# Performance work log

Measured on AMD Instinct MI355X. Metric: run time of the kernel, lower is better.

## Reference

```python
import jax, jax.numpy as jnp
import numpy as np

NEG_SLOPE = 0.2


def gat_conv(x, src, dst, W, a_src, a_dst, bias, heads, out_ch):
    # x: [N, F_in]; src/dst: [E] (message flows src -> dst, softmax over dst)
    N = x.shape[0]
    h = (x @ W).reshape(N, heads, out_ch)              # [N, H, C]
    alpha_s = (h * a_src).sum(-1)                      # [N, H]
    alpha_d = (h * a_dst).sum(-1)                      # [N, H]
    e = jax.nn.leaky_relu(alpha_s[src] + alpha_d[dst], NEG_SLOPE)  # [E, H]
    # segment softmax over destination nodes (every node has a self loop)
    emax = jax.ops.segment_max(e, dst, num_segments=N)             # [N, H]
    ee = jnp.exp(e - emax[dst])
    denom = jax.ops.segment_sum(ee, dst, num_segments=N)           # [N, H]
    alpha = ee / denom[dst]                                        # [E, H]
    msg = h[src] * alpha[..., None]                                # [E, H, C]
    out = jax.ops.segment_sum(msg, dst, num_segments=N)            # [N, H, C]
    return out.reshape(N, heads * out_ch) + bias


def setup_inputs() -> dict:
    key = jax.random.key(0)
    ks = jax.random.split(key, 12)
    N, E, EL = 100000, 1600000, 100000
    F_in, C, H = 128, 64, 2
    glorot = lambda k, shp: jax.random.normal(k, shp, jnp.float32) * np.sqrt(2.0 / (shp[0] + shp[-1]))
    return {
        "x": jax.random.normal(ks[0], (N, F_in), jnp.float32),
        "edge_index": jax.random.randint(ks[1], (2, E), 0, N, jnp.int32),
        "edge_label_index": jax.random.randint(ks[2], (2, EL), 0, N, jnp.int32),
        "W1": glorot(ks[3], (F_in, H * C)),
        "a_src1": glorot(ks[4], (H, C)),
        "a_dst1": glorot(ks[5], (H, C)),
        "b1": jnp.zeros((H * C,), jnp.float32),
        "W2": glorot(ks[6], (H * C, C)),
        "a_src2": glorot(ks[7], (1, C)),
        "a_dst2": glorot(ks[8], (1, C)),
        "b2": jnp.zeros((C,), jnp.float32),
    }


def reference(x, edge_index, edge_label_index, W1, a_src1, a_dst1, b1, W2, a_src2, a_dst2, b2):
    N = x.shape[0]
    # add self loops (PyG GATConv default)
    loop = jnp.arange(N, dtype=edge_index.dtype)
    src = jnp.concatenate([edge_index[0], loop])
    dst = jnp.concatenate([edge_index[1], loop])
    H, C = a_src1.shape[0], a_src1.shape[1]
    z = jax.nn.elu(gat_conv(x, src, dst, W1, a_src1, a_dst1, b1, H, C))
    z = gat_conv(z, src, dst, W2, a_src2, a_dst2, b2, 1, C)         # [N, C]
    # decode: dot product of endpoint embeddings
    return (z[edge_label_index[0]] * z[edge_label_index[1]]).sum(axis=1)
```

## Files before the change

kernel.cpp:

```cpp
#include <hip/hip_runtime.h>
#include <hip/hip_bf16.h>

#define NEG_SLOPE 0.2f
#define LRELU(v) ((v) > 0.f ? (v) : NEG_SLOPE * (v))
#define BBITS 7
#define BSZ 128
#define BCAP 3072

typedef unsigned short ushort_t;
typedef unsigned int uint_t;
typedef float v2f __attribute__((ext_vector_type(2)));
typedef float f32x4 __attribute__((ext_vector_type(4)));
typedef short bf16x8 __attribute__((ext_vector_type(8)));

static inline int cdiv(int a, int b) { return (a + b - 1) / b; }

__device__ __forceinline__ float wsum(float v) {
#pragma unroll
    for (int o = 32; o; o >>= 1) v += __shfl_xor(v, o);
    return v;
}
__device__ __forceinline__ ushort_t f2bfbits(float f) {
    __hip_bfloat16 b = __float2bfloat16(f);
    return *reinterpret_cast<ushort_t*>(&b);
}

__global__ __launch_bounds__(256) void k_init(int* __restrict__ bcur, int NB,
                                              const float* __restrict__ W1, ushort_t* __restrict__ Wt1,
                                              const float* __restrict__ W2, ushort_t* __restrict__ Wt2) {
    int idx = blockIdx.x * 256 + threadIdx.x;
    if (idx < NB) bcur[idx] = 0;
    if (idx < 128 * 128) {
        int k = idx >> 7, n = idx & 127;
        Wt1[n * 128 + k] = f2bfbits(W1[idx]);
    } else if (idx < 128 * 128 + 128 * 64) {
        int j = idx - 128 * 128;
        int k = j >> 6, n = j & 63;
        Wt2[n * 128 + k] = f2bfbits(W2[j]);
    }
}

__global__ __launch_bounds__(256) void k_bscatter(const int* __restrict__ ei, int E, int ET, int NB,
                                                  int* __restrict__ bcur,
                                                  uint_t* __restrict__ tmp) {
    extern __shared__ int sm2[];
    int* hist = sm2;
    int* cur = sm2 + NB;
    const int CH = 8192;
    int c0 = blockIdx.x * CH;
    int t = threadIdx.x;
    int dreg[32];
    for (int i = t; i < NB; i += 256) hist[i] = 0;
    __syncthreads();
#pragma unroll
    for (int j = 0; j < 32; j++) {
        int i = c0 + j * 256 + t;
        int d = -1;
        if (i < ET) d = (i < E) ? ei[E + i] : (i - E);
        dreg[j] = d;
        if (d >= 0) atomicAdd(&hist[d >> BBITS], 1);
    }
    __syncthreads();
    for (int i = t; i < NB; i += 256) {
        int c = hist[i];
        cur[i] = c ? atomicAdd(&bcur[i], c) : 0;
    }
    __syncthreads();
#pragma unroll
    for (int j = 0; j < 32; j++) {
        int i = c0 + j * 256 + t;
        int d = dreg[j];
        if (d >= 0) {
            int s = (i < E) ? ei[i] : (i - E);
            int b = d >> BBITS;
            int pos = atomicAdd(&cur[b], 1);
            pos = min(pos, BCAP - 1);
            tmp[(size_t)b * BCAP + pos] = ((uint_t)(d & (BSZ - 1)) << 25) | (uint_t)s;
        }
    }
}

__global__ __launch_bounds__(256) void k_csrfin(const uint_t* __restrict__ tmp,
                                                const int* __restrict__ bcnt, int NB, int N, int ET,
                                                int* __restrict__ offs, int* __restrict__ ssrc) {
    __shared__ int deg[BSZ], cur[BSZ], sc[BSZ], red[256];
    int b = blockIdx.x;
    int t = threadIdx.x;
    int part = 0;
    for (int i = t; i < b; i += 256) part += bcnt[i];
    red[t] = part;
    __syncthreads();
    for (int o = 128; o; o >>= 1) {
        if (t < o) red[t] += red[t + o];
        __syncthreads();
    }
    int r0 = red[0];
    int cnt = min(bcnt[b], BCAP);
    int node0 = b << BBITS;
    int nn = min(BSZ, N - node0);
    const uint_t* tb = tmp + (size_t)b * BCAP;
    if (t < BSZ) deg[t] = 0;
    if (b == 0 && t == 0) offs[N] = ET;
    __syncthreads();
    for (int j = t; j < cnt; j += 256) {
        int dloc = (int)(tb[j] >> 25);
        atomicAdd(&deg[dloc], 1);
    }
    __syncthreads();
    if (t < BSZ) sc[t] = deg[t];
    __syncthreads();
    for (int o = 1; o < BSZ; o <<= 1) {
        int v = 0;
        if (t < BSZ && t >= o) v = sc[t - o];
        __syncthreads();
        if (t < BSZ) sc[t] += v;
        __syncthreads();
    }
    if (t < BSZ) {
        int ex = sc[t] - deg[t];
        cur[t] = r0 + ex;
        if (t < nn) offs[node0 + t] = r0 + ex;
    }
    __syncthreads();
    for (int j = t; j < cnt; j += 256) {
        uint_t v = tb[j];
        int dloc = (int)(v >> 25);
        int s = (int)(v & 0x1FFFFFFu);
        int pos = atomicAdd(&cur[dloc], 1);
        ssrc[pos] = s;
    }
}

template <int M, int H, bool INBF16>
__global__ __launch_bounds__(256) void k_gemm_mfma(const void* __restrict__ xin,
                                                   const ushort_t* __restrict__ Wt,
                                                   const float* __restrict__ a_src,
                                                   const float* __restrict__ a_dst,
                                                   ushort_t* __restrict__ h,
                                                   float* __restrict__ as, float* __restrict__ ad,
                                                   int N) {
    constexpr int T = M / 16;
    int t = threadIdx.x;
    int w = t >> 6;
    int lane = t & 63;
    int ln = lane & 15;
    int q = lane >> 4;
    int rowA = blockIdx.x * 64 + w * 16 + ln;
    int rowD0 = blockIdx.x * 64 + w * 16 + q * 4;

    f32x4 acc[T];
#pragma unroll
    for (int i = 0; i < T; i++) acc[i] = (f32x4){0.f, 0.f, 0.f, 0.f};

#pragma unroll
    for (int kc = 0; kc < 4; kc++) {
        bf16x8 afrag;
        if (INBF16) {
            if (rowA < N)
                afrag = *(const bf16x8*)((const ushort_t*)xin + (size_t)rowA * 128 + kc * 32 + q * 8);
            else
#pragma unroll
                for (int j = 0; j < 8; j++) afrag[j] = 0;
        } else {
            float xv[8];
            if (rowA < N) {
                const float* xf = (const float*)xin;
                float4 v0 = *(const float4*)(xf + (size_t)rowA * 128 + kc * 32 + q * 8);
                float4 v1 = *(const float4*)(xf + (size_t)rowA * 128 + kc * 32 + q * 8 + 4);
                xv[0] = v0.x; xv[1] = v0.y; xv[2] = v0.z; xv[3] = v0.w;
                xv[4] = v1.x; xv[5] = v1.y; xv[6] = v1.z; xv[7] = v1.w;
            } else {
#pragma unroll
                for (int j = 0; j < 8; j++) xv[j] = 0.f;
            }
#pragma unroll
            for (int j = 0; j < 8; j++) afrag[j] = (short)f2bfbits(xv[j]);
        }
#pragma unroll
        for (int tt = 0; tt < T; tt++) {
            bf16x8 bfrag = *(const bf16x8*)(Wt + (size_t)(tt * 16 + ln) * 128 + kc * 32 + q * 8);
            acc[tt] = __builtin_amdgcn_mfma_f32_16x16x32_bf16(afrag, bfrag, acc[tt], 0, 0, 0);
        }
    }

#pragma unroll
    for (int tt = 0; tt < T; tt++)
#pragma unroll
        for (int r = 0; r < 4; r++) {
            int row = rowD0 + r;
            if (row < N) h[(size_t)row * M + tt * 16 + ln] = f2bfbits(acc[tt][r]);
        }

    float avs[T], avd[T];
#pragma unroll
    for (int tt = 0; tt < T; tt++) {
        avs[tt] = a_src[tt * 16 + ln];
        avd[tt] = a_dst[tt * 16 + ln];
    }
#pragma unroll
    for (int r = 0; r < 4; r++) {
        int row = rowD0 + r;
        if (H == 2) {
            float ps0 = 0.f, ps1 = 0.f, pd0 = 0.f, pd1 = 0.f;
#pragma unroll
            for (int tt = 0; tt < T / 2; tt++) { ps0 += acc[tt][r] * avs[tt]; pd0 += acc[tt][r] * avd[tt]; }
#pragma unroll
            for (int tt = T / 2; tt < T; tt++) { ps1 += acc[tt][r] * avs[tt]; pd1 += acc[tt][r] * avd[tt]; }
#pragma unroll
            for (int o = 8; o; o >>= 1) {
                ps0 += __shfl_down(ps0, o, 16); pd0 += __shfl_down(pd0, o, 16);
                ps1 += __shfl_down(ps1, o, 16); pd1 += __shfl_down(pd1, o, 16);
            }
            if (ln == 0 && row < N) {
                as[(size_t)row * 2] = ps0; as[(size_t)row * 2 + 1] = ps1;
                ad[(size_t)row * 2] = pd0; ad[(size_t)row * 2 + 1] = pd1;
            }
        } else {
            float ps = 0.f, pd = 0.f;
#pragma unroll
            for (int tt = 0; tt < T; tt++) { ps += acc[tt][r] * avs[tt]; pd += acc[tt][r] * avd[tt]; }
#pragma unroll
            for (int o = 8; o; o >>= 1) {
                ps += __shfl_down(ps, o, 16); pd += __shfl_down(pd, o, 16);
            }
            if (ln == 0 && row < N) { as[row] = ps; ad[row] = pd; }
        }
    }
}

template <int H, bool ELU_ACT, bool OUT_BF16>
__global__ __launch_bounds__(256) void k_agg_fused(const int* __restrict__ offs,
                                                   const int* __restrict__ ssrc,
                                                   const float* __restrict__ as,
                                                   const float* __restrict__ ad,
                                                   const ushort_t* __restrict__ h,
                                                   const float* __restrict__ bias,
                                                   void* __restrict__ z, int N) {
    constexpr int G = 16 * H;
    constexpr int EPW = 64 / G;
    constexpr int RB = H * 128;
    __shared__ __align__(16) uint2 lmeta[4][64 * H];
    int wv = threadIdx.x >> 6;
    int lane = threadIdx.x & 63;
    int d = (blockIdx.x * 256 + threadIdx.x) >> 6;
    if (d >= N) return;
    uint2* mw = lmeta[wv];
    int cpos = lane % G;
    int sub = lane / G;
    int hself = (H == 2) ? (cpos >> 4) : 0;
    const char* hb = (const char*)h;
    int cpo8 = cpos * 8;
    const char* mbase = (const char*)mw + ((H == 2) ? (sub * 16 + hself * 8) : (sub * 8));

    float adh0 = ad[(size_t)d * H];
    float adh1 = (H == 2) ? ad[(size_t)d * H + 1] : 0.f;
    float denp[2] = {0.f, 0.f};
    v2f acc2[2];
    acc2[0] = (v2f){0.f, 0.f};
    acc2[1] = (v2f){0.f, 0.f};

    int e0 = offs[d], e1 = offs[d + 1];
    for (int cb = e0; cb < e1; cb += 64) {
        int ne = min(64, e1 - cb);
        unsigned so = 0;
        float p0 = 0.f, p1 = 0.f;
        if (lane < ne) {
            int s_l = ssrc[cb + lane];
            so = (unsigned)s_l * RB;
            if (H == 2) {
                float2 av = ((const float2*)as)[s_l];
                p0 = __expf(LRELU(av.x + adh0));
                p1 = __expf(LRELU(av.y + adh1));
            } else {
                p0 = __expf(LRELU(as[s_l] + adh0));
            }
        }
        denp[0] += p0;
        denp[1] += p1;
        if (H == 2) {
            ((uint4*)mw)[lane] = make_uint4(so, __float_as_uint(p0), so, __float_as_uint(p1));
        } else {
            mw[lane] = make_uint2(so, __float_as_uint(p0));
        }
        int ng = (ne + EPW - 1) / EPW;
        for (int g0 = 0; g0 < ng; g0 += 4) {
            uint2 m[4];
#pragma unroll
            for (int g = 0; g < 4; g++) m[g] = *(const uint2*)(mbase + (g0 + g) * 32);
            uint2 hv[4];
#pragma unroll
            for (int g = 0; g < 4; g++) hv[g] = *(const uint2*)(hb + (m[g].x + cpo8));
#pragma unroll
            for (int g = 0; g < 4; g++) {
                float pvs = __uint_as_float(m[g].y);
                v2f pv = {pvs, pvs};
                v2f t0 = {__uint_as_float(hv[g].x << 16), __uint_as_float(hv[g].x & 0xffff0000u)};
                v2f t1 = {__uint_as_float(hv[g].y << 16), __uint_as_float(hv[g].y & 0xffff0000u)};
                acc2[0] += pv * t0;
                acc2[1] += pv * t1;
            }
        }
    }
#pragma unroll
    for (int o = G; o < 64; o <<= 1) {
        acc2[0][0] += __shfl_xor(acc2[0][0], o);
        acc2[0][1] += __shfl_xor(acc2[0][1], o);
        acc2[1][0] += __shfl_xor(acc2[1][0], o);
        acc2[1][1] += __shfl_xor(acc2[1][1], o);
    }
    float den0 = wsum(denp[0]);
    float den1 = (H == 2) ? wsum(denp[1]) : den0;
    if (lane < G) {
        float inv = 1.f / ((H == 2 && hself) ? den1 : den0);
        float vout[4];
        vout[0] = acc2[0][0] * inv + bias[cpos * 4 + 0];
        vout[1] = acc2[0][1] * inv + bias[cpos * 4 + 1];
        vout[2] = acc2[1][0] * inv + bias[cpos * 4 + 2];
        vout[3] = acc2[1][1] * inv + bias[cpos * 4 + 3];
        if (ELU_ACT) {
#pragma unroll
            for (int i = 0; i < 4; i++) vout[i] = vout[i] > 0.f ? vout[i] : expm1f(vout[i]);
        }
        if (OUT_BF16) {
            ushort4 pk;
            pk.x = f2bfbits(vout[0]); pk.y = f2bfbits(vout[1]);
            pk.z = f2bfbits(vout[2]); pk.w = f2bfbits(vout[3]);
            *(ushort4*)((ushort_t*)z + (size_t)d * (H * 64) + cpos * 4) = pk;
        } else {
            *(float4*)((float*)z + (size_t)d * (H * 64) + cpos * 4) =
                make_float4(vout[0], vout[1], vout[2], vout[3]);
        }
    }
}

__global__ __launch_bounds__(256) void k_decode(const int* __restrict__ eli,
                                                const ushort_t* __restrict__ z,
                                                float* __restrict__ out, int EL) {
    int wid = (blockIdx.x * 256 + threadIdx.x) >> 6;
    int lane = threadIdx.x & 63;
    int pi = wid * 4 + (lane >> 4);
    if (pi >= EL) return;
    int hl = lane & 15;
    int a = eli[pi], b = eli[EL + pi];
    uint2 ua = *(const uint2*)(z + (size_t)a * 64 + hl * 4);
    uint2 ub = *(const uint2*)(z + (size_t)b * 64 + hl * 4);
    float p = __uint_as_float(ua.x << 16) * __uint_as_float(ub.x << 16) +
              __uint_as_float(ua.x & 0xffff0000u) * __uint_as_float(ub.x & 0xffff0000u) +
              __uint_as_float(ua.y << 16) * __uint_as_float(ub.y << 16) +
              __uint_as_float(ua.y & 0xffff0000u) * __uint_as_float(ub.y & 0xffff0000u);
#pragma unroll
    for (int o = 8; o; o >>= 1) p += __shfl_down(p, o, 16);
    if (hl == 0) out[pi] = p;
}

extern "C" void kernel_launch(void* const* d_in, const int* in_sizes, int n_in,
                              void* d_out, int out_size, void* d_ws, size_t ws_size,
                              hipStream_t stream) {
    const float* x   = (const float*)d_in[0];
    const int*   ei  = (const int*)d_in[1];
    const int*   eli = (const int*)d_in[2];
    const float* W1  = (const float*)d_in[3];
    const float* as1 = (const float*)d_in[4];
    const float* ad1 = (const float*)d_in[5];
    const float* b1  = (const float*)d_in[6];
    const float* W2  = (const float*)d_in[7];
    const float* as2 = (const float*)d_in[8];
    const float* ad2 = (const float*)d_in[9];
    const float* b2  = (const float*)d_in[10];

    int N  = in_sizes[0] / 128;
    int E  = in_sizes[1] / 2;
    int EL = in_sizes[2] / 2;
    int ET = E + N;
    int NB = cdiv(N, BSZ);

    char* ws = (char*)d_ws;
    size_t off = 0;
    auto alloc = [&](size_t nbytes) -> void* {
        void* p = ws + off;
        off += (nbytes + 255) & ~(size_t)255;
        return p;
    };
    ushort_t* Hbuf = (ushort_t*)alloc((size_t)N * 128 * 2);
    char*     Zbuf = (char*)alloc((size_t)N * 128 * 2);
    float*    AS   = (float*)alloc((size_t)N * 2 * 4);
    float*    AD   = (float*)alloc((size_t)N * 2 * 4);
    int*      OFF  = (int*)alloc((size_t)(N + 1) * 4);
    int*      SSRC = (int*)alloc((size_t)ET * 4);
    int*      BCUR = (int*)alloc((size_t)NB * 4);
    ushort_t* WT1  = (ushort_t*)alloc(128 * 128 * 2);
    ushort_t* WT2  = (ushort_t*)alloc(64 * 128 * 2);
    uint_t*   TMP  = (uint_t*)Zbuf;

    k_init<<<cdiv(128 * 128 + 128 * 64, 256), 256, 0, stream>>>(BCUR, NB, W1, WT1, W2, WT2);
    k_bscatter<<<cdiv(ET, 8192), 256, 2 * NB * 4, stream>>>(ei, E, ET, NB, BCUR, TMP);
    k_csrfin<<<NB, 256, 0, stream>>>(TMP, BCUR, NB, N, ET, OFF, SSRC);

    k_gemm_mfma<128, 2, false><<<cdiv(N, 64), 256, 0, stream>>>(x, WT1, as1, ad1, Hbuf, AS, AD, N);
    k_agg_fused<2, true, true><<<cdiv(N, 4), 256, 0, stream>>>(OFF, SSRC, AS, AD, Hbuf, b1, Zbuf, N);

    k_gemm_mfma<64, 1, true><<<cdiv(N, 64), 256, 0, stream>>>(Zbuf, WT2, as2, ad2, Hbuf, AS, AD, N);
    k_agg_fused<1, false, true><<<cdiv(N, 4), 256, 0, stream>>>(OFF, SSRC, AS, AD, Hbuf, b2, Zbuf, N);

    k_decode<<<cdiv(EL, 16), 256, 0, stream>>>(eli, (const ushort_t*)Zbuf, (float*)d_out, EL);
}
```

Baseline: 324.1 us.

## Merge edge bucket scatter and layer-1 GEMM into one heterogeneous launch

Combines the bucket-scatter kernel and the first-layer MFMA GEMM into a single launch in which the first blocks do the scatter and the remaining blocks do the GEMM. The two are independent, so they can run concurrently and one launch plus one serialization point disappears. In exchange, the GEMM blocks now reserve the scatter's dynamic shared memory and may carry higher register pressure, which can lower occupancy for the GEMM portion.

Result: faster. 303.5 us, median of 2 (-6.3%).

```diff
diff --git a/kernel.cpp b/kernel.cpp
--- a/kernel.cpp
+++ b/kernel.cpp
@@ -40,14 +40,13 @@
     }
 }
 
-__global__ __launch_bounds__(256) void k_bscatter(const int* __restrict__ ei, int E, int ET, int NB,
-                                                  int* __restrict__ bcur,
-                                                  uint_t* __restrict__ tmp) {
-    extern __shared__ int sm2[];
+__device__ __forceinline__ void bscatter_body(int bb, const int* __restrict__ ei, int E, int ET,
+                                              int NB, int* __restrict__ bcur,
+                                              uint_t* __restrict__ tmp, int* sm2) {
     int* hist = sm2;
     int* cur = sm2 + NB;
     const int CH = 8192;
-    int c0 = blockIdx.x * CH;
+    int c0 = bb * CH;
     int t = threadIdx.x;
     int dreg[32];
     for (int i = t; i < NB; i += 256) hist[i] = 0;
@@ -80,73 +79,21 @@
     }
 }
 
-__global__ __launch_bounds__(256) void k_csrfin(const uint_t* __restrict__ tmp,
-                                                const int* __restrict__ bcnt, int NB, int N, int ET,
-                                                int* __restrict__ offs, int* __restrict__ ssrc) {
-    __shared__ int deg[BSZ], cur[BSZ], sc[BSZ], red[256];
-    int b = blockIdx.x;
-    int t = threadIdx.x;
-    int part = 0;
-    for (int i = t; i < b; i += 256) part += bcnt[i];
-    red[t] = part;
-    __syncthreads();
-    for (int o = 128; o; o >>= 1) {
-        if (t < o) red[t] += red[t + o];
-        __syncthreads();
-    }
-    int r0 = red[0];
-    int cnt = min(bcnt[b], BCAP);
-    int node0 = b << BBITS;
-    int nn = min(BSZ, N - node0);
-    const uint_t* tb = tmp + (size_t)b * BCAP;
-    if (t < BSZ) deg[t] = 0;
-    if (b == 0 && t == 0) offs[N] = ET;
-    __syncthreads();
-    for (int j = t; j < cnt; j += 256) {
-        int dloc = (int)(tb[j] >> 25);
-        atomicAdd(&deg[dloc], 1);
-    }
-    __syncthreads();
-    if (t < BSZ) sc[t] = deg[t];
-    __syncthreads();
-    for (int o = 1; o < BSZ; o <<= 1) {
-        int v = 0;
-        if (t < BSZ && t >= o) v = sc[t - o];
-        __syncthreads();
-        if (t < BSZ) sc[t] += v;
-        __syncthreads();
-    }
-    if (t < BSZ) {
-        int ex = sc[t] - deg[t];
-        cur[t] = r0 + ex;
-        if (t < nn) offs[node0 + t] = r0 + ex;
-    }
-    __syncthreads();
-    for (int j = t; j < cnt; j += 256) {
-        uint_t v = tb[j];
-        int dloc = (int)(v >> 25);
-        int s = (int)(v & 0x1FFFFFFu);
-        int pos = atomicAdd(&cur[dloc], 1);
-        ssrc[pos] = s;
-    }
-}
-
 template <int M, int H, bool INBF16>
-__global__ __launch_bounds__(256) void k_gemm_mfma(const void* __restrict__ xin,
-                                                   const ushort_t* __restrict__ Wt,
-                                                   const float* __restrict__ a_src,
-                                                   const float* __restrict__ a_dst,
-                                                   ushort_t* __restrict__ h,
-                                                   float* __restrict__ as, float* __restrict__ ad,
-                                                   int N) {
+__device__ __forceinline__ void gemm_body(int bid, const void* __restrict__ xin,
+                                          const ushort_t* __restrict__ Wt,
+                                          const float* __restrict__ a_src,
+                                          const float* __restrict__ a_dst,
+                                          ushort_t* __restrict__ h,
+                                          float* __restrict__ as, float* __restrict__ ad, int N) {
     constexpr int T = M / 16;
     int t = threadIdx.x;
     int w = t >> 6;
     int lane = t & 63;
     int ln = lane & 15;
     int q = lane >> 4;
-    int rowA = blockIdx.x * 64 + w * 16 + ln;
-    int rowD0 = blockIdx.x * 64 + w * 16 + q * 4;
+    int rowA = bid * 64 + w * 16 + ln;
+    int rowD0 = bid * 64 + w * 16 + q * 4;
 
     f32x4 acc[T];
 #pragma unroll
@@ -225,6 +172,85 @@
             }
             if (ln == 0 && row < N) { as[row] = ps; ad[row] = pd; }
         }
+    }
+}
+
+__global__ __launch_bounds__(256) void k_bsc_gemm(const int* __restrict__ ei, int E, int ET,
+                                                  int NB, int nbsc,
+                                                  int* __restrict__ bcur, uint_t* __restrict__ tmp,
+                                                  const float* __restrict__ x,
+                                                  const ushort_t* __restrict__ Wt1,
+                                                  const float* __restrict__ as1,
+                                                  const float* __restrict__ ad1,
+                                                  ushort_t* __restrict__ h,
+                                                  float* __restrict__ as, float* __restrict__ ad,
+                                                  int N) {
+    extern __shared__ int sm2[];
+    if (blockIdx.x < nbsc)
+        bscatter_body(blockIdx.x, ei, E, ET, NB, bcur, tmp, sm2);
+    else
+        gemm_body<128, 2, false>(blockIdx.x - nbsc, x, Wt1, as1, ad1, h, as, ad, N);
+}
+
+template <int M, int H, bool INBF16>
+__global__ __launch_bounds__(256) void k_gemm_mfma(const void* __restrict__ xin,
+                                                   const ushort_t* __restrict__ Wt,
+                                                   const float* __restrict__ a_src,
+                                                   const float* __restrict__ a_dst,
+                                                   ushort_t* __restrict__ h,
+                                                   float* __restrict__ as, float* __restrict__ ad,
+                                                   int N) {
+    gemm_body<M, H, INBF16>(blockIdx.x, xin, Wt, a_src, a_dst, h, as, ad, N);
+}
+
+__global__ __launch_bounds__(256) void k_csrfin(const uint_t* __restrict__ tmp,
+                                                const int* __restrict__ bcnt, int NB, int N, int ET,
+                                                int* __restrict__ offs, int* __restrict__ ssrc) {
+    __shared__ int deg[BSZ], cur[BSZ], sc[BSZ], red[256];
+    int b = blockIdx.x;
+    int t = threadIdx.x;
+    int part = 0;
+    for (int i = t; i < b; i += 256) part += bcnt[i];
+    red[t] = part;
+    __syncthreads();
+    for (int o = 128; o; o >>= 1) {
+        if (t < o) red[t] += red[t + o];
+        __syncthreads();
+    }
+    int r0 = red[0];
+    int cnt = min(bcnt[b], BCAP);
+    int node0 = b << BBITS;
+    int nn = min(BSZ, N - node0);
+    const uint_t* tb = tmp + (size_t)b * BCAP;
+    if (t < BSZ) deg[t] = 0;
+    if (b == 0 && t == 0) offs[N] = ET;
+    __syncthreads();
+    for (int j = t; j < cnt; j += 256) {
+        int dloc = (int)(tb[j] >> 25);
+        atomicAdd(&deg[dloc], 1);
+    }
+    __syncthreads();
+    if (t < BSZ) sc[t] = deg[t];
+    __syncthreads();
+    for (int o = 1; o < BSZ; o <<= 1) {
+        int v = 0;
+        if (t < BSZ && t >= o) v = sc[t - o];
+        __syncthreads();
+        if (t < BSZ) sc[t] += v;
+        __syncthreads();
+    }
+    if (t < BSZ) {
+        int ex = sc[t] - deg[t];
+        cur[t] = r0 + ex;
+        if (t < nn) offs[node0 + t] = r0 + ex;
+    }
+    __syncthreads();
+    for (int j = t; j < cnt; j += 256) {
+        uint_t v = tb[j];
+        int dloc = (int)(v >> 25);
+        int s = (int)(v & 0x1FFFFFFu);
+        int pos = atomicAdd(&cur[dloc], 1);
+        ssrc[pos] = s;
     }
 }
 
@@ -392,11 +418,15 @@
     ushort_t* WT2  = (ushort_t*)alloc(64 * 128 * 2);
     uint_t*   TMP  = (uint_t*)Zbuf;
 
+    int nbsc = cdiv(ET, 8192);
+
     k_init<<<cdiv(128 * 128 + 128 * 64, 256), 256, 0, stream>>>(BCUR, NB, W1, WT1, W2, WT2);
-    k_bscatter<<<cdiv(ET, 8192), 256, 2 * NB * 4, stream>>>(ei, E, ET, NB, BCUR, TMP);
+
+    k_bsc_gemm<<<nbsc + cdiv(N, 64), 256, 2 * NB * 4, stream>>>(
+        ei, E, ET, NB, nbsc, BCUR, TMP, x, WT1, as1, ad1, Hbuf, AS, AD, N);
+
     k_csrfin<<<NB, 256, 0, stream>>>(TMP, BCUR, NB, N, ET, OFF, SSRC);
 
-    k_gemm_mfma<128, 2, false><<<cdiv(N, 64), 256, 0, stream>>>(x, WT1, as1, ad1, Hbuf, AS, AD, N);
     k_agg_fused<2, true, true><<<cdiv(N, 4), 256, 0, stream>>>(OFF, SSRC, AS, AD, Hbuf, b1, Zbuf, N);
 
     k_gemm_mfma<64, 1, true><<<cdiv(N, 64), 256, 0, stream>>>(Zbuf, WT2, as2, ad2, Hbuf, AS, AD, N);
```
